# Optimization experiments

Hardware: AMD Instinct MI355X
Metric: run time of the kernel (lower is better)

The kernel has to match this reference:

```python
import jax, jax.numpy as jnp
import numpy as np

# TT factorization: vocab = 8*8*8*8*16 = 65536, dim = 4^5 = 1024, rank 16
SHAPE = [(8, 4), (8, 4), (8, 4), (8, 4), (16, 4)]
RANKS = [1, 16, 16, 16, 16, 1]
VOCAB = 65536
DIM = 1024
BATCH, SEQ = 8, 2048


def setup_inputs() -> dict:
    key = jax.random.key(0)
    ks = jax.random.split(key, len(SHAPE) + 1)
    inp = {}
    for k, (n, m) in enumerate(SHAPE):
        core = jax.random.normal(ks[k], (RANKS[k], n * m, RANKS[k + 1]), dtype=jnp.float32) * 0.01
        inp[f"core{k}"] = core
    inp["indices"] = jax.random.randint(ks[-1], (BATCH, SEQ), 0, VOCAB)
    return inp


def _tt_full(cores):
    # Faithful port of tt_to_matrix: chain matmul of cores, then a flat reshape
    # to (VOCAB, DIM).  (The original code reshapes merged_shape -> (rows, cols)
    # directly, without the inverse interleave permute; we replicate that.)
    result = cores[0]  # (1, n0*m0, r1)
    for core in cores[1:]:
        r_prev = result.shape[-1]
        result = (result.reshape(-1, r_prev) @ core.reshape(r_prev, -1))
        result = result.reshape(1, -1, core.shape[-1])
    return result.reshape(VOCAB, DIM)


def reference(core0, core1, core2, core3, core4, indices):
    full = _tt_full([core0, core1, core2, core3, core4])  # (VOCAB, DIM)
    return jnp.take(full, indices, axis=0)              # (BATCH, SEQ, DIM)
```

## Files before the change

### kernel.cpp

```cpp
#include <hip/hip_runtime.h>
#include <hip/hip_bf16.h>


#define RSTRIDE 20
#define GSTRIDE 328

__global__ __launch_bounds__(256, 8) void tt_embed_kernel(
    const float* __restrict__ c0,
    const float* __restrict__ c1,
    const float* __restrict__ c2,
    const float* __restrict__ c3,
    const float* __restrict__ c4,
    const int*   __restrict__ idx,
    float*       __restrict__ out,
    int n_tokens)
{
    const int t   = threadIdx.x;
    const int tl  = t >> 5;
    const int l32 = t & 31;
    const int r   = t & 15;
    const int l   = t & 63;
    const int wid = t >> 6;
    const int token = blockIdx.x * 8 + tl;
    const int v = (token < n_tokens) ? idx[token] : 0;

    __shared__ float w4s[8 * GSTRIDE];

    float c4v[16];
    #pragma unroll
    for (int r4 = 0; r4 < 16; ++r4)
        c4v[r4] = c4[(r4 << 6) + l];

    float w2r = 0.f;
    {
        const int i0 = (v >> 11) & 31;
        const int i1 = (v >> 6) & 31;
        #pragma unroll
        for (int r1 = 0; r1 < 16; ++r1)
            w2r = fmaf(c0[i0 * 16 + r1], c1[(r1 * 32 + i1) * 16 + r], w2r);
    }

    float w3r = 0.f;
    {
        const int i2 = (v >> 1) & 31;
        #pragma unroll
        for (int r2 = 0; r2 < 16; ++r2)
            w3r = fmaf(__shfl(w2r, r2, 16), c2[(r2 * 32 + i2) * 16 + r], w3r);
    }

    {
        const int vlow16 = (v & 1) << 4;
        float4 a0 = {0,0,0,0}, a1 = {0,0,0,0};
        #pragma unroll
        for (int r3 = 0; r3 < 16; ++r3) {
            const float wv = __shfl(w3r, r3, 16);
            const float* base = c3 + ((r3 * 32 + vlow16) << 4);
            const float4 b0 = *(const float4*)(base + (l32 << 2));
            const float4 b1 = *(const float4*)(base + 128 + (l32 << 2));
            a0.x = fmaf(wv, b0.x, a0.x); a0.y = fmaf(wv, b0.y, a0.y);
            a0.z = fmaf(wv, b0.z, a0.z); a0.w = fmaf(wv, b0.w, a0.w);
            a1.x = fmaf(wv, b1.x, a1.x); a1.y = fmaf(wv, b1.y, a1.y);
            a1.z = fmaf(wv, b1.z, a1.z); a1.w = fmaf(wv, b1.w, a1.w);
        }
        float* sb = &w4s[tl * GSTRIDE + ((l32 & 3) << 2)];
        *(float4*)(sb + ((l32 >> 2)    ) * RSTRIDE) = a0;
        *(float4*)(sb + (8 + (l32 >> 2)) * RSTRIDE) = a1;
    }

    #pragma unroll
    for (int s = 0; s < 2; ++s) {
        const int slot = 2 * wid + s;
        const int tok  = blockIdx.x * 8 + slot;
        const float* slab = &w4s[slot * GSTRIDE];
        float* outp = out + (size_t)tok * 1024 + l;

        #pragma unroll
        for (int k = 0; k < 16; ++k) {
            const float4* wp = (const float4*)(slab + k * RSTRIDE);
            const float4 wa = wp[0], wb = wp[1], wc = wp[2], wd = wp[3];

            float acc = 0.f;
            acc = fmaf(wa.x, c4v[ 0], acc);
            acc = fmaf(wa.y, c4v[ 1], acc);
            acc = fmaf(wa.z, c4v[ 2], acc);
            acc = fmaf(wa.w, c4v[ 3], acc);
            acc = fmaf(wb.x, c4v[ 4], acc);
            acc = fmaf(wb.y, c4v[ 5], acc);
            acc = fmaf(wb.z, c4v[ 6], acc);
            acc = fmaf(wb.w, c4v[ 7], acc);
            acc = fmaf(wc.x, c4v[ 8], acc);
            acc = fmaf(wc.y, c4v[ 9], acc);
            acc = fmaf(wc.z, c4v[10], acc);
            acc = fmaf(wc.w, c4v[11], acc);
            acc = fmaf(wd.x, c4v[12], acc);
            acc = fmaf(wd.y, c4v[13], acc);
            acc = fmaf(wd.z, c4v[14], acc);
            acc = fmaf(wd.w, c4v[15], acc);

            if (tok < n_tokens)
                __builtin_nontemporal_store(acc, outp + (k << 6));
        }
    }
}

extern "C" void kernel_launch(void* const* d_in, const int* in_sizes, int n_in,
                              void* d_out, int out_size, void* d_ws, size_t ws_size,
                              hipStream_t stream) {
    const float* c0  = (const float*)d_in[0];
    const float* c1  = (const float*)d_in[1];
    const float* c2  = (const float*)d_in[2];
    const float* c3  = (const float*)d_in[3];
    const float* c4  = (const float*)d_in[4];
    const int*   idx = (const int*)d_in[5];
    float* out = (float*)d_out;

    const int n_tokens = in_sizes[5];
    const int grid = (n_tokens + 7) / 8;
    tt_embed_kernel<<<grid, 256, 0, stream>>>(c0, c1, c2, c3, c4, idx, out, n_tokens);
}
```

Baseline: 26.59 us.

## Vectorize output stores to float4 and replace shuffles with LDS broadcasts

The final contraction is remapped so each lane computes four consecutive output columns. It holds float4 slices of core4 and issues 128-bit nontemporal stores, replacing scalar 32-bit stores. The rank-vector broadcasts for the w2 and w3 stages now go through small shared-memory buffers read as float4, instead of 16 cross-lane shuffles each. The occupancy hint in launch_bounds is dropped; with 64 floats of core4 now held per lane, register pressure rises and occupancy may fall.

```diff
diff --git a/kernel.cpp b/kernel.cpp
--- a/kernel.cpp
+++ b/kernel.cpp
@@ -2,10 +2,12 @@
 #include <hip/hip_bf16.h>
 
 
+typedef float f32x4 __attribute__((ext_vector_type(4)));
+
 #define RSTRIDE 20
 #define GSTRIDE 328
 
-__global__ __launch_bounds__(256, 8) void tt_embed_kernel(
+__global__ __launch_bounds__(256) void tt_embed_kernel(
     const float* __restrict__ c0,
     const float* __restrict__ c1,
     const float* __restrict__ c2,
@@ -25,35 +27,57 @@
     const int v = (token < n_tokens) ? idx[token] : 0;
 
     __shared__ float w4s[8 * GSTRIDE];
+    __shared__ float w2b[8][20];
+    __shared__ float w3b[8][20];
 
-    float c4v[16];
+    float4 c4v[16];
     #pragma unroll
     for (int r4 = 0; r4 < 16; ++r4)
-        c4v[r4] = c4[(r4 << 6) + l];
+        c4v[r4] = *(const float4*)(c4 + (r4 << 6) + ((l & 15) << 2));
 
-    float w2r = 0.f;
     {
         const int i0 = (v >> 11) & 31;
         const int i1 = (v >> 6) & 31;
+        float w2r = 0.f;
         #pragma unroll
         for (int r1 = 0; r1 < 16; ++r1)
             w2r = fmaf(c0[i0 * 16 + r1], c1[(r1 * 32 + i1) * 16 + r], w2r);
+        w2b[tl][r] = w2r;
     }
 
-    float w3r = 0.f;
+    float4 w2v[4];
+    #pragma unroll
+    for (int q = 0; q < 4; ++q)
+        w2v[q] = *(const float4*)&w2b[tl][q << 2];
+
     {
         const int i2 = (v >> 1) & 31;
+        float w3r = 0.f;
         #pragma unroll
-        for (int r2 = 0; r2 < 16; ++r2)
-            w3r = fmaf(__shfl(w2r, r2, 16), c2[(r2 * 32 + i2) * 16 + r], w3r);
+        for (int q = 0; q < 4; ++q) {
+            w3r = fmaf(w2v[q].x, c2[((q * 4 + 0) * 32 + i2) * 16 + r], w3r);
+            w3r = fmaf(w2v[q].y, c2[((q * 4 + 1) * 32 + i2) * 16 + r], w3r);
+            w3r = fmaf(w2v[q].z, c2[((q * 4 + 2) * 32 + i2) * 16 + r], w3r);
+            w3r = fmaf(w2v[q].w, c2[((q * 4 + 3) * 32 + i2) * 16 + r], w3r);
+        }
+        w3b[tl][r] = w3r;
     }
+
+    float4 w3v[4];
+    #pragma unroll
+    for (int q = 0; q < 4; ++q)
+        w3v[q] = *(const float4*)&w3b[tl][q << 2];
 
     {
         const int vlow16 = (v & 1) << 4;
         float4 a0 = {0,0,0,0}, a1 = {0,0,0,0};
+        const float wv_arr0[16] = {w3v[0].x, w3v[0].y, w3v[0].z, w3v[0].w,
+                                   w3v[1].x, w3v[1].y, w3v[1].z, w3v[1].w,
+                                   w3v[2].x, w3v[2].y, w3v[2].z, w3v[2].w,
+                                   w3v[3].x, w3v[3].y, w3v[3].z, w3v[3].w};
         #pragma unroll
         for (int r3 = 0; r3 < 16; ++r3) {
-            const float wv = __shfl(w3r, r3, 16);
+            const float wv = wv_arr0[r3];
             const float* base = c3 + ((r3 * 32 + vlow16) << 4);
             const float4 b0 = *(const float4*)(base + (l32 << 2));
             const float4 b1 = *(const float4*)(base + 128 + (l32 << 2));
@@ -72,33 +96,33 @@
         const int slot = 2 * wid + s;
         const int tok  = blockIdx.x * 8 + slot;
         const float* slab = &w4s[slot * GSTRIDE];
-        float* outp = out + (size_t)tok * 1024 + l;
+        const int sub = l >> 4;
+        const int colb = (l & 15) << 2;
 
         #pragma unroll
-        for (int k = 0; k < 16; ++k) {
-            const float4* wp = (const float4*)(slab + k * RSTRIDE);
-            const float4 wa = wp[0], wb = wp[1], wc = wp[2], wd = wp[3];
+        for (int j = 0; j < 4; ++j) {
+            const int row = (j << 2) + sub;
+            const float* rp = slab + row * RSTRIDE;
+            const float4 wa = *(const float4*)(rp);
+            const float4 wb = *(const float4*)(rp + 4);
+            const float4 wc = *(const float4*)(rp + 8);
+            const float4 wd = *(const float4*)(rp + 12);
 
-            float acc = 0.f;
-            acc = fmaf(wa.x, c4v[ 0], acc);
-            acc = fmaf(wa.y, c4v[ 1], acc);
-            acc = fmaf(wa.z, c4v[ 2], acc);
-            acc = fmaf(wa.w, c4v[ 3], acc);
-            acc = fmaf(wb.x, c4v[ 4], acc);
-            acc = fmaf(wb.y, c4v[ 5], acc);
-            acc = fmaf(wb.z, c4v[ 6], acc);
-            acc = fmaf(wb.w, c4v[ 7], acc);
-            acc = fmaf(wc.x, c4v[ 8], acc);
-            acc = fmaf(wc.y, c4v[ 9], acc);
-            acc = fmaf(wc.z, c4v[10], acc);
-            acc = fmaf(wc.w, c4v[11], acc);
-            acc = fmaf(wd.x, c4v[12], acc);
-            acc = fmaf(wd.y, c4v[13], acc);
-            acc = fmaf(wd.z, c4v[14], acc);
-            acc = fmaf(wd.w, c4v[15], acc);
+            float4 acc = {0,0,0,0};
+            #define FMA4(WV, k)                          \
+                acc.x = fmaf(WV, c4v[k].x, acc.x);       \
+                acc.y = fmaf(WV, c4v[k].y, acc.y);       \
+                acc.z = fmaf(WV, c4v[k].z, acc.z);       \
+                acc.w = fmaf(WV, c4v[k].w, acc.w);
+            FMA4(wa.x,  0) FMA4(wa.y,  1) FMA4(wa.z,  2) FMA4(wa.w,  3)
+            FMA4(wb.x,  4) FMA4(wb.y,  5) FMA4(wb.z,  6) FMA4(wb.w,  7)
+            FMA4(wc.x,  8) FMA4(wc.y,  9) FMA4(wc.z, 10) FMA4(wc.w, 11)
+            FMA4(wd.x, 12) FMA4(wd.y, 13) FMA4(wd.z, 14) FMA4(wd.w, 15)
+            #undef FMA4
 
             if (tok < n_tokens)
-                __builtin_nontemporal_store(acc, outp + (k << 6));
+                __builtin_nontemporal_store(*(const f32x4*)&acc,
+                    (f32x4*)(out + (size_t)tok * 1024 + (row << 6) + colb));
         }
     }
 }
```

Measured after the change: 25.59 us. 3.8% less time.
